# Kernel tuning notes

Hardware: AMD Instinct MI355X
Metric: run time of the kernel (lower is better)

## Reference

```python
import jax, jax.numpy as jnp
import numpy as np

B, N, F, K, FILT = 256, 256, 128, 4, 256  # batch mols, max_atom, Fin, Chebyshev order, nb_filter
EPS = float(np.spacing(np.float32(0)))    # matches np.spacing(0) in original degree normalization
D2_FLOOR = 1e-12                          # numerical floor for sqrt of pairwise sq-dist


def setup_inputs() -> dict:
    key = jax.random.key(0)
    ks = jax.random.split(key, 6)
    x = jax.random.normal(ks[0], (B, N, F), dtype=jnp.float32)
    lap_in = 0.1 * jax.random.normal(ks[1], (B, N, N), dtype=jnp.float32)  # input per-mol Laplacian
    n_atoms = jax.random.randint(ks[2], (B,), 64, N + 1, dtype=jnp.int32)  # ragged mol sizes
    r1 = float(np.sqrt(6.0 / (F + F)))
    M_L = jax.random.uniform(ks[3], (F, F), jnp.float32, -r1, r1)          # Mahalanobis metric
    r2 = float(np.sqrt(6.0 / (F * K + FILT)))
    weight = jax.random.uniform(ks[4], (F * K, FILT), jnp.float32, -r2, r2)
    bias = jnp.zeros((FILT,), jnp.float32)
    return {"x": x, "lap_in": lap_in, "n_atoms": n_atoms, "M_L": M_L, "weight": weight, "bias": bias}


def reference(x, lap_in, n_atoms, M_L, weight, bias):
    # mask[b,n] = 1 for real atoms, 0 for padding (replaces per-mol tf.slice + pad)
    mask = (jnp.arange(N)[None, :] < n_atoms[:, None]).astype(x.dtype)       # [B,N]
    x = x * mask[..., None]

    # ---- learned Laplacian: Mahalanobis RBF affinity + sym degree normalization ----
    xw = jnp.einsum('bnf,fg->bng', x, M_L)                                   # x @ M_L
    sq = jnp.sum(xw * xw, axis=-1)                                           # [B,N]
    d2 = sq[:, :, None] + sq[:, None, :] - 2.0 * jnp.einsum('bif,bjf->bij', xw, xw)
    eye = jnp.eye(N, dtype=x.dtype)
    off = mask[:, :, None] * mask[:, None, :] * (1.0 - eye)                  # valid off-diag pairs
    d2_safe = jnp.where(off > 0, jnp.maximum(d2, D2_FLOOR), 1.0)
    W = jnp.exp(-jnp.sqrt(d2_safe)) * off                                    # W[i,j]=exp(-dist), diag 0
    deg = jnp.sum(W, axis=1) + EPS                                           # W symmetric: axis0==axis1
    dinv = jnp.where(mask > 0, 1.0 / jnp.sqrt(deg), 0.0)                     # D^{-1/2} (0 on padding)
    # L = I - D^{-1/2} W D^{-1/2} (intended math of the original py_func)
    L_learn = eye[None] * mask[:, :, None] - dinv[:, :, None] * W * dinv[:, None, :]
    L = L_learn + lap_in * (mask[:, :, None] * mask[:, None, :])             # L + sliced input LL

    # ---- Chebyshev recurrence: x0=x, x1=Lx, xk = 2 L x_{k-1} - x_{k-2} ----
    x0 = x
    x1 = jnp.einsum('bij,bjf->bif', L, x0)
    xs = [x0, x1]
    for _ in range(2, K):
        x2 = 2.0 * jnp.einsum('bij,bjf->bif', L, x1) - x0
        xs.append(x2)
        x0, x1 = x1, x2
    # stack -> [B,N,F,K] then flatten (f,k) row-major, matching reshape([K,M,F])->transpose([1,2,0])->reshape([M,K*F])
    xc = jnp.stack(xs, axis=-1).reshape(B, N, F * K)

    out = jnp.einsum('bnd,do->bno', xc, weight) + bias                       # [B,N,FILT]
    out = jax.nn.relu(out * mask[..., None])                                 # pad-to-max_atom + relu
    return out, L_learn
```

## Files before the change

### kernel.cpp

```cpp
#include <hip/hip_runtime.h>
#include <math.h>

typedef __bf16 bf16;
typedef __bf16 bf16x8 __attribute__((ext_vector_type(8)));
typedef __bf16 bf16x4 __attribute__((ext_vector_type(4)));
typedef float f32x4 __attribute__((ext_vector_type(4)));

constexpr int cB = 256, cN = 256, cF = 128, cO = 256;
constexpr int BN = cB * cN;
constexpr float D2_FLOOR = 1e-12f;
constexpr float EPS_F = 1.401298464324817e-45f;

constexpr size_t OFF_XC  = 0;
constexpr size_t OFF_W   = OFF_XC + (size_t)BN * 512 * 2;
constexpr size_t OFF_X0T = OFF_W + (size_t)cB * cN * cN * 4;
constexpr size_t OFF_X1T = OFF_X0T + (size_t)cB * cF * cN * 2;
constexpr size_t OFF_LB  = OFF_X1T + (size_t)cB * cF * cN * 2;
constexpr size_t OFF_WT  = OFF_LB + (size_t)cB * cN * cN * 2;
constexpr size_t OFF_MT  = OFF_WT + 512 * 256 * 2;
constexpr size_t OFF_SQ  = OFF_MT + 128 * 128 * 2;
constexpr size_t OFF_DI  = OFF_SQ + (size_t)BN * 4;

__device__ __forceinline__ void gll16(const void* g, void* l) {
  __builtin_amdgcn_global_load_lds((const __attribute__((address_space(1))) void*)g,
                                   (__attribute__((address_space(3))) void*)l, 16, 0, 0);
}

template<int NWAVE>
__device__ __forceinline__ void stage_panel(const bf16* __restrict__ src, int ld,
                                            int nrf, int k0, char* lds,
                                            int wid, int lane) {
  const bf16* g0 = src + (size_t)(lane & 15) * ld + k0 + 8 * (lane >> 4);
  const int nIss = nrf * 2;
  for (int u = wid; u < nIss; u += NWAVE) {
    int rf = u >> 1, ks = u & 1;
    gll16(g0 + (size_t)rf * 16 * ld + ks * 32, lds + (u << 10));
  }
}

template<int NF>
__device__ __forceinline__ void mfma_chunk(const char* Al, const char* Bl, int lane,
                                           f32x4 acc[8][NF]) {
#pragma unroll
  for (int ks = 0; ks < 2; ++ks) {
    bf16x8 a[8];
#pragma unroll
    for (int mf = 0; mf < 8; ++mf)
      a[mf] = *(const bf16x8*)(Al + ((mf * 2 + ks) << 10) + lane * 16);
#pragma unroll
    for (int nf = 0; nf < NF; ++nf) {
      bf16x8 b = *(const bf16x8*)(Bl + ((nf * 2 + ks) << 10) + lane * 16);
#pragma unroll
      for (int mf = 0; mf < 8; ++mf)
        acc[mf][nf] = __builtin_amdgcn_mfma_f32_16x16x32_bf16(a[mf], b, acc[mf][nf], 0, 0, 0);
    }
  }
}

__global__ __launch_bounds__(256) void k_prep(const float* __restrict__ x,
                                              const int* __restrict__ na_p,
                                              bf16* __restrict__ xc,
                                              bf16* __restrict__ x0T) {
  __shared__ __align__(16) bf16 T[64][132];
  int b = blockIdx.x >> 2, i0 = (blockIdx.x & 3) * 64;
  int tid = threadIdx.x;
  int na = na_p[b];
#pragma unroll
  for (int it = 0; it < 8; ++it) {
    int ir = it * 8 + (tid >> 5);
    int f0 = (tid & 31) * 4;
    int i = i0 + ir;
    float m = (i < na) ? 1.f : 0.f;
    float4 v = *(const float4*)(x + ((size_t)b * cN + i) * cF + f0);
    bf16x4 pk = {(bf16)(v.x * m), (bf16)(v.y * m), (bf16)(v.z * m), (bf16)(v.w * m)};
    *(bf16x4*)(xc + ((size_t)b * cN + i) * 512 + f0) = pk;
    *(bf16x4*)(&T[ir][f0]) = pk;
  }
  __syncthreads();
  int f = tid >> 1, half = tid & 1;
  bf16* od = x0T + ((size_t)b * cF + f) * cN + i0 + half * 32;
#pragma unroll
  for (int c = 0; c < 32; c += 4) {
    int ii = half * 32 + c;
    bf16x4 pk = {T[ii][f], T[ii + 1][f], T[ii + 2][f], T[ii + 3][f]};
    *(bf16x4*)(od + c) = pk;
  }
}

__global__ __launch_bounds__(256) void k_wt(const float* __restrict__ wgt,
                                            const float* __restrict__ ML,
                                            bf16* __restrict__ Wt,
                                            bf16* __restrict__ MT) {
  int id = blockIdx.x * 256 + threadIdx.x;
  if (id < 512 * 256) {
    int o = id >> 9, d = id & 511;
    int k = d >> 7, f = d & 127;
    Wt[id] = (bf16)wgt[(f * 4 + k) * 256 + o];
  } else {
    int id2 = id - 512 * 256;
    if (id2 < 128 * 128) {
      int g = id2 >> 7, f = id2 & 127;
      MT[id2] = (bf16)ML[f * 128 + g];
    }
  }
}

__global__ __launch_bounds__(256, 1) void k_xw_mfma(const bf16* __restrict__ xc,
                                                    const bf16* __restrict__ MT,
                                                    bf16* __restrict__ xw) {
  __shared__ __align__(16) char AL[2][16384];
  __shared__ __align__(16) char BL[2][16384];
  int tid = threadIdx.x, wid = tid >> 6, lane = tid & 63;
  int r0 = blockIdx.x * 128;
  const bf16* A = xc + (size_t)r0 * 512;
  f32x4 acc[8][2] = {};
  stage_panel<4>(A, 512, 8, 0, AL[0], wid, lane);
  stage_panel<4>(MT, 128, 8, 0, BL[0], wid, lane);
  __syncthreads();
#pragma unroll
  for (int kc = 0; kc < 2; ++kc) {
    if (kc < 1) {
      stage_panel<4>(A, 512, 8, 64, AL[1], wid, lane);
      stage_panel<4>(MT, 128, 8, 64, BL[1], wid, lane);
    }
    mfma_chunk<2>(AL[kc], BL[kc] + wid * 4096, lane, acc);
    __syncthreads();
  }
  int r4 = 4 * (lane >> 4), il = lane & 15;
#pragma unroll
  for (int mf = 0; mf < 8; ++mf)
#pragma unroll
    for (int nf = 0; nf < 2; ++nf)
#pragma unroll
      for (int r = 0; r < 4; ++r) {
        int row = r0 + mf * 16 + r4 + r;
        int g = wid * 32 + nf * 16 + il;
        xw[(size_t)row * cF + g] = (bf16)acc[mf][nf][r];
      }
}

__global__ __launch_bounds__(256) void k_sq(const bf16* __restrict__ xw,
                                            float* __restrict__ sq) {
  int tid = threadIdx.x, lane = tid & 63;
  int row = blockIdx.x * 4 + (tid >> 6);
  const bf16* p = xw + (size_t)row * cF + lane * 2;
  float a = (float)p[0], b2 = (float)p[1];
  float s = a * a + b2 * b2;
#pragma unroll
  for (int o = 32; o; o >>= 1) s += __shfl_down(s, o);
  if (lane == 0) sq[row] = s;
}

__global__ __launch_bounds__(512, 1) void k_gram_mfma(const bf16* __restrict__ xw,
                                                      const float* __restrict__ sq,
                                                      const int* __restrict__ na_p,
                                                      float* __restrict__ Wb) {
  __shared__ __align__(16) char P[2][32768];
  __shared__ float lsq[256];
  int b = blockIdx.x;
  int tid = threadIdx.x, wid = tid >> 6, lane = tid & 63;
  const bf16* X = xw + (size_t)b * cN * cF;
  int wm = wid >> 2, wn = wid & 3;
  f32x4 acc[8][4] = {};
  stage_panel<8>(X, cF, 16, 0, P[0], wid, lane);
  if (tid < 256) lsq[tid] = sq[b * cN + tid];
  __syncthreads();
#pragma unroll
  for (int kc = 0; kc < 2; ++kc) {
    if (kc < 1) stage_panel<8>(X, cF, 16, 64, P[1], wid, lane);
    mfma_chunk<4>(P[kc] + wm * 16384, P[kc] + wn * 8192, lane, acc);
    __syncthreads();
  }
  int na = na_p[b];
  int r4 = 4 * (lane >> 4), il = lane & 15;
  float* Wrow = Wb + (size_t)b * cN * cN;
#pragma unroll
  for (int mf = 0; mf < 8; ++mf)
#pragma unroll
    for (int nf = 0; nf < 4; ++nf) {
      int j = wn * 64 + nf * 16 + il;
      float sqj = lsq[j];
      bool mj = j < na;
#pragma unroll
      for (int r = 0; r < 4; ++r) {
        int i = wm * 128 + mf * 16 + r4 + r;
        float w = 0.f;
        if (mj && i < na && i != j) {
          float d2 = fmaxf(lsq[i] + sqj - 2.f * acc[mf][nf][r], D2_FLOOR);
          w = expf(-sqrtf(d2));
        }
        Wrow[(size_t)i * cN + j] = w;
      }
    }
}

__global__ __launch_bounds__(256) void k_dinv(const float* __restrict__ Wb,
                                              const int* __restrict__ na_p,
                                              float* __restrict__ dinv) {
  int tid = threadIdx.x, lane = tid & 63;
  int row = blockIdx.x * 4 + (tid >> 6);
  float4 v = *(const float4*)(Wb + (size_t)row * cN + lane * 4);
  float s = v.x + v.y + v.z + v.w;
#pragma unroll
  for (int o = 32; o; o >>= 1) s += __shfl_down(s, o);
  if (lane == 0) {
    int b = row >> 8, n = row & 255;
    dinv[row] = (n < na_p[b]) ? 1.f / sqrtf(s + EPS_F) : 0.f;
  }
}

__global__ __launch_bounds__(256) void k_L(const float* __restrict__ lap,
                                           const int* __restrict__ na_p,
                                           const float* __restrict__ dinv,
                                           const float* __restrict__ Wb,
                                           bf16* __restrict__ Lb,
                                           float* __restrict__ llearn) {
  size_t e = ((size_t)blockIdx.x * 256 + threadIdx.x) * 4;
  int j = (int)(e & 255);
  int i = (int)((e >> 8) & 255);
  int b = (int)(e >> 16);
  float4 w = *(const float4*)(Wb + e);
  float4 lp = *(const float4*)(lap + e);
  float di = dinv[b * cN + i];
  const float* djp = dinv + b * cN + j;
  int na = na_p[b];
  float mi = (i < na) ? 1.f : 0.f;
  float4 ll;
  bf16x4 lo;
#pragma unroll
  for (int c = 0; c < 4; ++c) {
    float v = -di * (&w.x)[c] * djp[c];
    if (i == j + c && i < na) v += 1.f;
    (&ll.x)[c] = v;
    float mj = (j + c < na) ? 1.f : 0.f;
    lo[c] = (bf16)(v + (&lp.x)[c] * mi * mj);
  }
  *(float4*)(llearn + e) = ll;
  *(bf16x4*)(Lb + e) = lo;
}

template<bool BETA, bool WRITE_T>
__global__ __launch_bounds__(256, 1) void k_cheb_mfma(const bf16* __restrict__ xT,
                                                      const bf16* __restrict__ Lb,
                                                      const bf16* __restrict__ xppT,
                                                      bf16* __restrict__ xoutT,
                                                      bf16* __restrict__ xc, int kcol) {
  __shared__ __align__(16) char AL[2][16384];
  __shared__ __align__(16) char BL[2][32768];
  int b = blockIdx.x;
  int tid = threadIdx.x, wid = tid >> 6, lane = tid & 63;
  const bf16* A = xT + (size_t)b * cF * cN;
  const bf16* Bm = Lb + (size_t)b * cN * cN;
  f32x4 acc[8][4] = {};
  stage_panel<4>(A, cN, 8, 0, AL[0], wid, lane);
  stage_panel<4>(Bm, cN, 16, 0, BL[0], wid, lane);
  __syncthreads();
#pragma unroll
  for (int kc = 0; kc < 4; ++kc) {
    int cur = kc & 1;
    if (kc < 3) {
      stage_panel<4>(A, cN, 8, (kc + 1) * 64, AL[cur ^ 1], wid, lane);
      stage_panel<4>(Bm, cN, 16, (kc + 1) * 64, BL[cur ^ 1], wid, lane);
    }
    mfma_chunk<4>(AL[cur], BL[cur] + wid * 8192, lane, acc);
    __syncthreads();
  }
  int i0 = wid * 64;
  int r4 = 4 * (lane >> 4), il = lane & 15;
#pragma unroll
  for (int mf = 0; mf < 8; ++mf)
#pragma unroll
    for (int nf = 0; nf < 4; ++nf) {
      int i = i0 + nf * 16 + il;
      int f0 = mf * 16 + r4;
      bf16x4 pk;
#pragma unroll
      for (int r = 0; r < 4; ++r) {
        float v = acc[mf][nf][r];
        if (BETA) v = 2.f * v - (float)xppT[(size_t)b * cF * cN + (size_t)(f0 + r) * cN + i];
        bf16 bv = (bf16)v;
        pk[r] = bv;
        if (WRITE_T) xoutT[(size_t)b * cF * cN + (size_t)(f0 + r) * cN + i] = bv;
      }
      *(bf16x4*)(xc + ((size_t)b * cN + i) * 512 + kcol + f0) = pk;
    }
}

__global__ __launch_bounds__(256, 1) void k_out_mfma(const bf16* __restrict__ xc,
                                                     const bf16* __restrict__ Wt,
                                                     const float* __restrict__ bias,
                                                     const int* __restrict__ na_p,
                                                     float* __restrict__ out) {
  __shared__ __align__(16) char AL[2][16384];
  __shared__ __align__(16) char BL[2][32768];
  int tid = threadIdx.x, wid = tid >> 6, lane = tid & 63;
  int r0 = blockIdx.x * 128;
  const bf16* A = xc + (size_t)r0 * 512;
  f32x4 acc[8][4] = {};
  stage_panel<4>(A, 512, 8, 0, AL[0], wid, lane);
  stage_panel<4>(Wt, 512, 16, 0, BL[0], wid, lane);
  __syncthreads();
  for (int kc = 0; kc < 8; ++kc) {
    int cur = kc & 1;
    if (kc < 7) {
      stage_panel<4>(A, 512, 8, (kc + 1) * 64, AL[cur ^ 1], wid, lane);
      stage_panel<4>(Wt, 512, 16, (kc + 1) * 64, BL[cur ^ 1], wid, lane);
    }
    mfma_chunk<4>(AL[cur], BL[cur] + wid * 8192, lane, acc);
    __syncthreads();
  }
  int na = na_p[r0 >> 8];
  int o0 = wid * 64;
  int r4 = 4 * (lane >> 4), il = lane & 15;
#pragma unroll
  for (int nf = 0; nf < 4; ++nf) {
    int o = o0 + nf * 16 + il;
    float bo = bias[o];
#pragma unroll
    for (int mf = 0; mf < 8; ++mf)
#pragma unroll
      for (int r = 0; r < 4; ++r) {
        int row = r0 + mf * 16 + r4 + r;
        float m = ((row & 255) < na) ? 1.f : 0.f;
        out[(size_t)row * cO + o] = fmaxf((acc[mf][nf][r] + bo) * m, 0.f);
      }
  }
}

extern "C" void kernel_launch(void* const* d_in, const int* in_sizes, int n_in,
                              void* d_out, int out_size, void* d_ws, size_t ws_size,
                              hipStream_t stream) {
  const float* x    = (const float*)d_in[0];
  const float* lap  = (const float*)d_in[1];
  const int*   na   = (const int*)d_in[2];
  const float* M_L  = (const float*)d_in[3];
  const float* wgt  = (const float*)d_in[4];
  const float* bias = (const float*)d_in[5];

  float* out    = (float*)d_out;
  float* llearn = out + (size_t)BN * cO;

  char* ws = (char*)d_ws;
  bf16*  xc  = (bf16*)(ws + OFF_XC);
  float* Wb  = (float*)(ws + OFF_W);
  bf16*  x2T = (bf16*)(ws + OFF_W);
  bf16*  x0T = (bf16*)(ws + OFF_X0T);
  bf16*  x1T = (bf16*)(ws + OFF_X1T);
  bf16*  xw  = (bf16*)(ws + OFF_X1T);
  bf16*  Lb  = (bf16*)(ws + OFF_LB);
  bf16*  Wt  = (bf16*)(ws + OFF_WT);
  bf16*  MT  = (bf16*)(ws + OFF_MT);
  float* sqb = (float*)(ws + OFF_SQ);
  float* dnv = (float*)(ws + OFF_DI);

  k_prep<<<dim3(1024), 256, 0, stream>>>(x, na, xc, x0T);
  k_wt<<<dim3(576), 256, 0, stream>>>(wgt, M_L, Wt, MT);
  k_xw_mfma<<<dim3(512), 256, 0, stream>>>(xc, MT, xw);
  k_sq<<<dim3(BN / 4), 256, 0, stream>>>(xw, sqb);
  k_gram_mfma<<<dim3(cB), 512, 0, stream>>>(xw, sqb, na, Wb);
  k_dinv<<<dim3(BN / 4), 256, 0, stream>>>(Wb, na, dnv);
  k_L<<<dim3(16384), 256, 0, stream>>>(lap, na, dnv, Wb, Lb, llearn);
  k_cheb_mfma<false, true><<<dim3(cB), 256, 0, stream>>>(x0T, Lb, x0T, x1T, xc, 128);
  k_cheb_mfma<true, true><<<dim3(cB), 256, 0, stream>>>(x1T, Lb, x0T, x2T, xc, 256);
  k_cheb_mfma<true, false><<<dim3(cB), 256, 0, stream>>>(x2T, Lb, x1T, x2T, xc, 384);
  k_out_mfma<<<dim3(512), 256, 0, stream>>>(xc, Wt, bias, na, out);
}
```

Measured before the change: 427.6 us.

## Fuse gram, degree and Laplacian kernels; drop LDS staging for direct global MFMA loads

Folds the squared-norm reduction into the xw GEMM and fuses the gram/RBF, degree, dinv and Laplacian construction into one per-molecule kernel. This removes the fp32 W buffer round trip through global memory and several launches. All GEMM kernels now load MFMA fragments straight from global memory instead of staging through LDS. The Chebyshev kernels are split into two blocks per molecule, with occupancy hints raised to 2. The trade-off is more uncoalesced, cache-dependent global loads and scalar bf16 stores into xc, and the fast __expf replaces expf.

Measured after the change: 432.9 us. About the same (+1.2%).

```diff
diff --git a/kernel.cpp b/kernel.cpp
--- a/kernel.cpp
+++ b/kernel.cpp
@@ -12,49 +12,22 @@
 constexpr float EPS_F = 1.401298464324817e-45f;
 
 constexpr size_t OFF_XC  = 0;
-constexpr size_t OFF_W   = OFF_XC + (size_t)BN * 512 * 2;
-constexpr size_t OFF_X0T = OFF_W + (size_t)cB * cN * cN * 4;
+constexpr size_t OFF_XW  = OFF_XC + (size_t)BN * 512 * 2;
+constexpr size_t OFF_X0T = OFF_XW + (size_t)BN * 128 * 2;
 constexpr size_t OFF_X1T = OFF_X0T + (size_t)cB * cF * cN * 2;
-constexpr size_t OFF_LB  = OFF_X1T + (size_t)cB * cF * cN * 2;
+constexpr size_t OFF_X2T = OFF_X1T + (size_t)cB * cF * cN * 2;
+constexpr size_t OFF_LB  = OFF_X2T + (size_t)cB * cF * cN * 2;
 constexpr size_t OFF_WT  = OFF_LB + (size_t)cB * cN * cN * 2;
 constexpr size_t OFF_MT  = OFF_WT + 512 * 256 * 2;
 constexpr size_t OFF_SQ  = OFF_MT + 128 * 128 * 2;
-constexpr size_t OFF_DI  = OFF_SQ + (size_t)BN * 4;
-
-__device__ __forceinline__ void gll16(const void* g, void* l) {
-  __builtin_amdgcn_global_load_lds((const __attribute__((address_space(1))) void*)g,
-                                   (__attribute__((address_space(3))) void*)l, 16, 0, 0);
-}
-
-template<int NWAVE>
-__device__ __forceinline__ void stage_panel(const bf16* __restrict__ src, int ld,
-                                            int nrf, int k0, char* lds,
-                                            int wid, int lane) {
-  const bf16* g0 = src + (size_t)(lane & 15) * ld + k0 + 8 * (lane >> 4);
-  const int nIss = nrf * 2;
-  for (int u = wid; u < nIss; u += NWAVE) {
-    int rf = u >> 1, ks = u & 1;
-    gll16(g0 + (size_t)rf * 16 * ld + ks * 32, lds + (u << 10));
-  }
-}
-
-template<int NF>
-__device__ __forceinline__ void mfma_chunk(const char* Al, const char* Bl, int lane,
-                                           f32x4 acc[8][NF]) {
-#pragma unroll
-  for (int ks = 0; ks < 2; ++ks) {
-    bf16x8 a[8];
-#pragma unroll
-    for (int mf = 0; mf < 8; ++mf)
-      a[mf] = *(const bf16x8*)(Al + ((mf * 2 + ks) << 10) + lane * 16);
-#pragma unroll
-    for (int nf = 0; nf < NF; ++nf) {
-      bf16x8 b = *(const bf16x8*)(Bl + ((nf * 2 + ks) << 10) + lane * 16);
-#pragma unroll
-      for (int mf = 0; mf < 8; ++mf)
-        acc[mf][nf] = __builtin_amdgcn_mfma_f32_16x16x32_bf16(a[mf], b, acc[mf][nf], 0, 0, 0);
-    }
-  }
+
+__device__ __forceinline__ bf16x8 gfrag(const bf16* __restrict__ p, int ld,
+                                        int lane, int k0) {
+  return *(const bf16x8*)(p + (size_t)(lane & 15) * ld + k0 + 8 * (lane >> 4));
+}
+
+__device__ __forceinline__ f32x4 mfma(bf16x8 a, bf16x8 b, f32x4 c) {
+  return __builtin_amdgcn_mfma_f32_16x16x32_bf16(a, b, c, 0, 0, 0);
 }
 
 __global__ __launch_bounds__(256) void k_prep(const float* __restrict__ x,
@@ -105,225 +78,217 @@
   }
 }
 
-__global__ __launch_bounds__(256, 1) void k_xw_mfma(const bf16* __restrict__ xc,
-                                                    const bf16* __restrict__ MT,
-                                                    bf16* __restrict__ xw) {
-  __shared__ __align__(16) char AL[2][16384];
-  __shared__ __align__(16) char BL[2][16384];
+__global__ __launch_bounds__(256, 2) void k_xw2(const bf16* __restrict__ xc,
+                                                const bf16* __restrict__ MT,
+                                                bf16* __restrict__ xw,
+                                                float* __restrict__ sq) {
+  __shared__ float sqb[128];
   int tid = threadIdx.x, wid = tid >> 6, lane = tid & 63;
   int r0 = blockIdx.x * 128;
   const bf16* A = xc + (size_t)r0 * 512;
+  const bf16* Bg = MT + (size_t)(wid * 32) * 128;
   f32x4 acc[8][2] = {};
-  stage_panel<4>(A, 512, 8, 0, AL[0], wid, lane);
-  stage_panel<4>(MT, 128, 8, 0, BL[0], wid, lane);
-  __syncthreads();
-#pragma unroll
-  for (int kc = 0; kc < 2; ++kc) {
-    if (kc < 1) {
-      stage_panel<4>(A, 512, 8, 64, AL[1], wid, lane);
-      stage_panel<4>(MT, 128, 8, 64, BL[1], wid, lane);
-    }
-    mfma_chunk<2>(AL[kc], BL[kc] + wid * 4096, lane, acc);
-    __syncthreads();
-  }
-  int r4 = 4 * (lane >> 4), il = lane & 15;
-#pragma unroll
-  for (int mf = 0; mf < 8; ++mf)
-#pragma unroll
-    for (int nf = 0; nf < 2; ++nf)
-#pragma unroll
-      for (int r = 0; r < 4; ++r) {
-        int row = r0 + mf * 16 + r4 + r;
-        int g = wid * 32 + nf * 16 + il;
-        xw[(size_t)row * cF + g] = (bf16)acc[mf][nf][r];
-      }
-}
-
-__global__ __launch_bounds__(256) void k_sq(const bf16* __restrict__ xw,
-                                            float* __restrict__ sq) {
-  int tid = threadIdx.x, lane = tid & 63;
-  int row = blockIdx.x * 4 + (tid >> 6);
-  const bf16* p = xw + (size_t)row * cF + lane * 2;
-  float a = (float)p[0], b2 = (float)p[1];
-  float s = a * a + b2 * b2;
-#pragma unroll
-  for (int o = 32; o; o >>= 1) s += __shfl_down(s, o);
-  if (lane == 0) sq[row] = s;
-}
-
-__global__ __launch_bounds__(512, 1) void k_gram_mfma(const bf16* __restrict__ xw,
-                                                      const float* __restrict__ sq,
-                                                      const int* __restrict__ na_p,
-                                                      float* __restrict__ Wb) {
-  __shared__ __align__(16) char P[2][32768];
+#pragma unroll
+  for (int ks = 0; ks < 4; ++ks) {
+    int k0 = ks * 32;
+    bf16x8 b0 = gfrag(Bg, 128, lane, k0);
+    bf16x8 b1 = gfrag(Bg + 16 * 128, 128, lane, k0);
+#pragma unroll
+    for (int mf = 0; mf < 8; ++mf) {
+      bf16x8 a = gfrag(A + (size_t)mf * 16 * 512, 512, lane, k0);
+      acc[mf][0] = mfma(a, b0, acc[mf][0]);
+      acc[mf][1] = mfma(a, b1, acc[mf][1]);
+    }
+  }
+  if (tid < 128) sqb[tid] = 0.f;
+  __syncthreads();
+  int hi = lane >> 4, il = lane & 15;
+#pragma unroll
+  for (int mf = 0; mf < 8; ++mf) {
+#pragma unroll
+    for (int r = 0; r < 4; ++r) {
+      int row = r0 + mf * 16 + 4 * hi + r;
+      float s = 0.f;
+#pragma unroll
+      for (int nf = 0; nf < 2; ++nf) {
+        bf16 v = (bf16)acc[mf][nf][r];
+        xw[(size_t)row * cF + wid * 32 + nf * 16 + il] = v;
+        float f = (float)v;
+        s = fmaf(f, f, s);
+      }
+      s += __shfl_xor(s, 1); s += __shfl_xor(s, 2);
+      s += __shfl_xor(s, 4); s += __shfl_xor(s, 8);
+      if (il == 0) atomicAdd(&sqb[mf * 16 + 4 * hi + r], s);
+    }
+  }
+  __syncthreads();
+  if (tid < 128) sq[r0 + tid] = sqb[tid];
+}
+
+__global__ __launch_bounds__(512, 2) void k_gramL(const bf16* __restrict__ xw,
+                                                  const float* __restrict__ sq,
+                                                  const float* __restrict__ lap,
+                                                  const int* __restrict__ na_p,
+                                                  bf16* __restrict__ Lb,
+                                                  float* __restrict__ llearn) {
   __shared__ float lsq[256];
-  int b = blockIdx.x;
-  int tid = threadIdx.x, wid = tid >> 6, lane = tid & 63;
+  __shared__ float deg[256];
+  __shared__ float dinv[256];
+  int b = blockIdx.x, tid = threadIdx.x, wid = tid >> 6, lane = tid & 63;
+  int wm = wid >> 2, wn = wid & 3;
+  if (tid < 256) { lsq[tid] = sq[b * cN + tid]; deg[tid] = 0.f; }
   const bf16* X = xw + (size_t)b * cN * cF;
-  int wm = wid >> 2, wn = wid & 3;
+  const bf16* Ag = X + (size_t)(wm * 128) * cF;
+  const bf16* Bg = X + (size_t)(wn * 64) * cF;
   f32x4 acc[8][4] = {};
-  stage_panel<8>(X, cF, 16, 0, P[0], wid, lane);
-  if (tid < 256) lsq[tid] = sq[b * cN + tid];
-  __syncthreads();
-#pragma unroll
-  for (int kc = 0; kc < 2; ++kc) {
-    if (kc < 1) stage_panel<8>(X, cF, 16, 64, P[1], wid, lane);
-    mfma_chunk<4>(P[kc] + wm * 16384, P[kc] + wn * 8192, lane, acc);
-    __syncthreads();
-  }
+#pragma unroll
+  for (int ks = 0; ks < 4; ++ks) {
+    int k0 = ks * 32;
+    bf16x8 bb[4];
+#pragma unroll
+    for (int nf = 0; nf < 4; ++nf) bb[nf] = gfrag(Bg + (size_t)nf * 16 * cF, cF, lane, k0);
+#pragma unroll
+    for (int mf = 0; mf < 8; ++mf) {
+      bf16x8 a = gfrag(Ag + (size_t)mf * 16 * cF, cF, lane, k0);
+#pragma unroll
+      for (int nf = 0; nf < 4; ++nf) acc[mf][nf] = mfma(a, bb[nf], acc[mf][nf]);
+    }
+  }
+  __syncthreads();
   int na = na_p[b];
-  int r4 = 4 * (lane >> 4), il = lane & 15;
-  float* Wrow = Wb + (size_t)b * cN * cN;
-#pragma unroll
-  for (int mf = 0; mf < 8; ++mf)
-#pragma unroll
-    for (int nf = 0; nf < 4; ++nf) {
-      int j = wn * 64 + nf * 16 + il;
-      float sqj = lsq[j];
-      bool mj = j < na;
-#pragma unroll
-      for (int r = 0; r < 4; ++r) {
-        int i = wm * 128 + mf * 16 + r4 + r;
+  int hi = lane >> 4, il = lane & 15;
+#pragma unroll
+  for (int mf = 0; mf < 8; ++mf) {
+#pragma unroll
+    for (int r = 0; r < 4; ++r) {
+      int i = wm * 128 + mf * 16 + 4 * hi + r;
+      float sqi = lsq[i];
+      bool mi = i < na;
+      float rs = 0.f;
+#pragma unroll
+      for (int nf = 0; nf < 4; ++nf) {
+        int j = wn * 64 + nf * 16 + il;
         float w = 0.f;
-        if (mj && i < na && i != j) {
-          float d2 = fmaxf(lsq[i] + sqj - 2.f * acc[mf][nf][r], D2_FLOOR);
-          w = expf(-sqrtf(d2));
+        if (mi && j < na && i != j) {
+          float d2 = fmaxf(sqi + lsq[j] - 2.f * acc[mf][nf][r], D2_FLOOR);
+          w = __expf(-sqrtf(d2));
         }
-        Wrow[(size_t)i * cN + j] = w;
-      }
-    }
-}
-
-__global__ __launch_bounds__(256) void k_dinv(const float* __restrict__ Wb,
-                                              const int* __restrict__ na_p,
-                                              float* __restrict__ dinv) {
-  int tid = threadIdx.x, lane = tid & 63;
-  int row = blockIdx.x * 4 + (tid >> 6);
-  float4 v = *(const float4*)(Wb + (size_t)row * cN + lane * 4);
-  float s = v.x + v.y + v.z + v.w;
-#pragma unroll
-  for (int o = 32; o; o >>= 1) s += __shfl_down(s, o);
-  if (lane == 0) {
-    int b = row >> 8, n = row & 255;
-    dinv[row] = (n < na_p[b]) ? 1.f / sqrtf(s + EPS_F) : 0.f;
-  }
-}
-
-__global__ __launch_bounds__(256) void k_L(const float* __restrict__ lap,
-                                           const int* __restrict__ na_p,
-                                           const float* __restrict__ dinv,
-                                           const float* __restrict__ Wb,
-                                           bf16* __restrict__ Lb,
-                                           float* __restrict__ llearn) {
-  size_t e = ((size_t)blockIdx.x * 256 + threadIdx.x) * 4;
-  int j = (int)(e & 255);
-  int i = (int)((e >> 8) & 255);
-  int b = (int)(e >> 16);
-  float4 w = *(const float4*)(Wb + e);
-  float4 lp = *(const float4*)(lap + e);
-  float di = dinv[b * cN + i];
-  const float* djp = dinv + b * cN + j;
-  int na = na_p[b];
-  float mi = (i < na) ? 1.f : 0.f;
-  float4 ll;
-  bf16x4 lo;
-#pragma unroll
-  for (int c = 0; c < 4; ++c) {
-    float v = -di * (&w.x)[c] * djp[c];
-    if (i == j + c && i < na) v += 1.f;
-    (&ll.x)[c] = v;
-    float mj = (j + c < na) ? 1.f : 0.f;
-    lo[c] = (bf16)(v + (&lp.x)[c] * mi * mj);
-  }
-  *(float4*)(llearn + e) = ll;
-  *(bf16x4*)(Lb + e) = lo;
+        acc[mf][nf][r] = w;
+        rs += w;
+      }
+      rs += __shfl_xor(rs, 1); rs += __shfl_xor(rs, 2);
+      rs += __shfl_xor(rs, 4); rs += __shfl_xor(rs, 8);
+      if (il == 0) atomicAdd(&deg[i], rs);
+    }
+  }
+  __syncthreads();
+  if (tid < 256) dinv[tid] = (tid < na) ? 1.f / sqrtf(deg[tid] + EPS_F) : 0.f;
+  __syncthreads();
+  const float* lapb = lap + (size_t)b * cN * cN;
+  float* llb = llearn + (size_t)b * cN * cN;
+  bf16* lbb = Lb + (size_t)b * cN * cN;
+#pragma unroll
+  for (int mf = 0; mf < 8; ++mf) {
+#pragma unroll
+    for (int r = 0; r < 4; ++r) {
+      int i = wm * 128 + mf * 16 + 4 * hi + r;
+      float di = dinv[i];
+      float mi = (i < na) ? 1.f : 0.f;
+#pragma unroll
+      for (int nf = 0; nf < 4; ++nf) {
+        int j = wn * 64 + nf * 16 + il;
+        float v = -di * acc[mf][nf][r] * dinv[j];
+        if (i == j && i < na) v += 1.f;
+        size_t e = (size_t)i * cN + j;
+        llb[e] = v;
+        float mj = (j < na) ? 1.f : 0.f;
+        lbb[e] = (bf16)(v + lapb[e] * mi * mj);
+      }
+    }
+  }
 }
 
 template<bool BETA, bool WRITE_T>
-__global__ __launch_bounds__(256, 1) void k_cheb_mfma(const bf16* __restrict__ xT,
-                                                      const bf16* __restrict__ Lb,
-                                                      const bf16* __restrict__ xppT,
-                                                      bf16* __restrict__ xoutT,
-                                                      bf16* __restrict__ xc, int kcol) {
-  __shared__ __align__(16) char AL[2][16384];
-  __shared__ __align__(16) char BL[2][32768];
-  int b = blockIdx.x;
+__global__ __launch_bounds__(256, 2) void k_cheb2(const bf16* __restrict__ xT,
+                                                  const bf16* __restrict__ Lb,
+                                                  const bf16* __restrict__ xppT,
+                                                  bf16* __restrict__ xoutT,
+                                                  bf16* __restrict__ xc, int kcol) {
+  int bx = blockIdx.x;
+  int b = bx >> 1, i0 = (bx & 1) * 128;
   int tid = threadIdx.x, wid = tid >> 6, lane = tid & 63;
   const bf16* A = xT + (size_t)b * cF * cN;
-  const bf16* Bm = Lb + (size_t)b * cN * cN;
-  f32x4 acc[8][4] = {};
-  stage_panel<4>(A, cN, 8, 0, AL[0], wid, lane);
-  stage_panel<4>(Bm, cN, 16, 0, BL[0], wid, lane);
-  __syncthreads();
-#pragma unroll
-  for (int kc = 0; kc < 4; ++kc) {
-    int cur = kc & 1;
-    if (kc < 3) {
-      stage_panel<4>(A, cN, 8, (kc + 1) * 64, AL[cur ^ 1], wid, lane);
-      stage_panel<4>(Bm, cN, 16, (kc + 1) * 64, BL[cur ^ 1], wid, lane);
-    }
-    mfma_chunk<4>(AL[cur], BL[cur] + wid * 8192, lane, acc);
-    __syncthreads();
-  }
-  int i0 = wid * 64;
-  int r4 = 4 * (lane >> 4), il = lane & 15;
-#pragma unroll
-  for (int mf = 0; mf < 8; ++mf)
-#pragma unroll
-    for (int nf = 0; nf < 4; ++nf) {
-      int i = i0 + nf * 16 + il;
-      int f0 = mf * 16 + r4;
-      bf16x4 pk;
+  const bf16* Bg = Lb + (size_t)b * cN * cN + (size_t)(i0 + wid * 32) * cN;
+  f32x4 acc[8][2] = {};
+#pragma unroll
+  for (int ks = 0; ks < 8; ++ks) {
+    int k0 = ks * 32;
+    bf16x8 b0 = gfrag(Bg, cN, lane, k0);
+    bf16x8 b1 = gfrag(Bg + 16 * cN, cN, lane, k0);
+#pragma unroll
+    for (int mf = 0; mf < 8; ++mf) {
+      bf16x8 a = gfrag(A + (size_t)mf * 16 * cN, cN, lane, k0);
+      acc[mf][0] = mfma(a, b0, acc[mf][0]);
+      acc[mf][1] = mfma(a, b1, acc[mf][1]);
+    }
+  }
+  int hi = lane >> 4, il = lane & 15;
+#pragma unroll
+  for (int mf = 0; mf < 8; ++mf) {
+#pragma unroll
+    for (int nf = 0; nf < 2; ++nf) {
+      int i = i0 + wid * 32 + nf * 16 + il;
 #pragma unroll
       for (int r = 0; r < 4; ++r) {
+        int f = mf * 16 + 4 * hi + r;
         float v = acc[mf][nf][r];
-        if (BETA) v = 2.f * v - (float)xppT[(size_t)b * cF * cN + (size_t)(f0 + r) * cN + i];
+        if (BETA) v = 2.f * v - (float)xppT[(size_t)b * cF * cN + (size_t)f * cN + i];
         bf16 bv = (bf16)v;
-        pk[r] = bv;
-        if (WRITE_T) xoutT[(size_t)b * cF * cN + (size_t)(f0 + r) * cN + i] = bv;
-      }
-      *(bf16x4*)(xc + ((size_t)b * cN + i) * 512 + kcol + f0) = pk;
-    }
-}
-
-__global__ __launch_bounds__(256, 1) void k_out_mfma(const bf16* __restrict__ xc,
-                                                     const bf16* __restrict__ Wt,
-                                                     const float* __restrict__ bias,
-                                                     const int* __restrict__ na_p,
-                                                     float* __restrict__ out) {
-  __shared__ __align__(16) char AL[2][16384];
-  __shared__ __align__(16) char BL[2][32768];
+        if (WRITE_T) xoutT[(size_t)b * cF * cN + (size_t)f * cN + i] = bv;
+        xc[((size_t)b * cN + i) * 512 + kcol + f] = bv;
+      }
+    }
+  }
+}
+
+__global__ __launch_bounds__(256, 2) void k_out2(const bf16* __restrict__ xc,
+                                                 const bf16* __restrict__ Wt,
+                                                 const float* __restrict__ bias,
+                                                 const int* __restrict__ na_p,
+                                                 float* __restrict__ out) {
   int tid = threadIdx.x, wid = tid >> 6, lane = tid & 63;
   int r0 = blockIdx.x * 128;
   const bf16* A = xc + (size_t)r0 * 512;
+  const bf16* Bg = Wt + (size_t)(wid * 64) * 512;
   f32x4 acc[8][4] = {};
-  stage_panel<4>(A, 512, 8, 0, AL[0], wid, lane);
-  stage_panel<4>(Wt, 512, 16, 0, BL[0], wid, lane);
-  __syncthreads();
-  for (int kc = 0; kc < 8; ++kc) {
-    int cur = kc & 1;
-    if (kc < 7) {
-      stage_panel<4>(A, 512, 8, (kc + 1) * 64, AL[cur ^ 1], wid, lane);
-      stage_panel<4>(Wt, 512, 16, (kc + 1) * 64, BL[cur ^ 1], wid, lane);
-    }
-    mfma_chunk<4>(AL[cur], BL[cur] + wid * 8192, lane, acc);
-    __syncthreads();
+#pragma unroll 4
+  for (int ks = 0; ks < 16; ++ks) {
+    int k0 = ks * 32;
+    bf16x8 bb[4];
+#pragma unroll
+    for (int nf = 0; nf < 4; ++nf) bb[nf] = gfrag(Bg + (size_t)nf * 16 * 512, 512, lane, k0);
+#pragma unroll
+    for (int mf = 0; mf < 8; ++mf) {
+      bf16x8 a = gfrag(A + (size_t)mf * 16 * 512, 512, lane, k0);
+#pragma unroll
+      for (int nf = 0; nf < 4; ++nf) acc[mf][nf] = mfma(a, bb[nf], acc[mf][nf]);
+    }
   }
   int na = na_p[r0 >> 8];
-  int o0 = wid * 64;
-  int r4 = 4 * (lane >> 4), il = lane & 15;
+  int hi = lane >> 4, il = lane & 15;
 #pragma unroll
   for (int nf = 0; nf < 4; ++nf) {
-    int o = o0 + nf * 16 + il;
+    int o = wid * 64 + nf * 16 + il;
     float bo = bias[o];
 #pragma unroll
-    for (int mf = 0; mf < 8; ++mf)
+    for (int mf = 0; mf < 8; ++mf) {
 #pragma unroll
       for (int r = 0; r < 4; ++r) {
-        int row = r0 + mf * 16 + r4 + r;
+        int row = r0 + mf * 16 + 4 * hi + r;
         float m = ((row & 255) < na) ? 1.f : 0.f;
         out[(size_t)row * cO + o] = fmaxf((acc[mf][nf][r] + bo) * m, 0.f);
       }
+    }
   }
 }
 
@@ -342,26 +307,21 @@
 
   char* ws = (char*)d_ws;
   bf16*  xc  = (bf16*)(ws + OFF_XC);
-  float* Wb  = (float*)(ws + OFF_W);
-  bf16*  x2T = (bf16*)(ws + OFF_W);
+  bf16*  xw  = (bf16*)(ws + OFF_XW);
   bf16*  x0T = (bf16*)(ws + OFF_X0T);
   bf16*  x1T = (bf16*)(ws + OFF_X1T);
-  bf16*  xw  = (bf16*)(ws + OFF_X1T);
+  bf16*  x2T = (bf16*)(ws + OFF_X2T);
   bf16*  Lb  = (bf16*)(ws + OFF_LB);
   bf16*  Wt  = (bf16*)(ws + OFF_WT);
   bf16*  MT  = (bf16*)(ws + OFF_MT);
   float* sqb = (float*)(ws + OFF_SQ);
-  float* dnv = (float*)(ws + OFF_DI);
 
   k_prep<<<dim3(1024), 256, 0, stream>>>(x, na, xc, x0T);
   k_wt<<<dim3(576), 256, 0, stream>>>(wgt, M_L, Wt, MT);
-  k_xw_mfma<<<dim3(512), 256, 0, stream>>>(xc, MT, xw);
-  k_sq<<<dim3(BN / 4), 256, 0, stream>>>(xw, sqb);
-  k_gram_mfma<<<dim3(cB), 512, 0, stream>>>(xw, sqb, na, Wb);
-  k_dinv<<<dim3(BN / 4), 256, 0, stream>>>(Wb, na, dnv);
-  k_L<<<dim3(16384), 256, 0, stream>>>(lap, na, dnv, Wb, Lb, llearn);
-  k_cheb_mfma<false, true><<<dim3(cB), 256, 0, stream>>>(x0T, Lb, x0T, x1T, xc, 128);
-  k_cheb_mfma<true, true><<<dim3(cB), 256, 0, stream>>>(x1T, Lb, x0T, x2T, xc, 256);
-  k_cheb_mfma<true, false><<<dim3(cB), 256, 0, stream>>>(x2T, Lb, x1T, x2T, xc, 384);
-  k_out_mfma<<<dim3(512), 256, 0, stream>>>(xc, Wt, bias, na, out);
-}
+  k_xw2<<<dim3(512), 256, 0, stream>>>(xc, MT, xw, sqb);
+  k_gramL<<<dim3(cB), 512, 0, stream>>>(xw, sqb, lap, na, Lb, llearn);
+  k_cheb2<false, true><<<dim3(512), 256, 0, stream>>>(x0T, Lb, x0T, x1T, xc, 128);
+  k_cheb2<true, true><<<dim3(512), 256, 0, stream>>>(x1T, Lb, x0T, x2T, xc, 256);
+  k_cheb2<true, false><<<dim3(512), 256, 0, stream>>>(x2T, Lb, x1T, x2T, xc, 384);
+  k_out2<<<dim3(512), 256, 0, stream>>>(xc, Wt, bias, na, out);
+}
```
